# Optimization experiments

Hardware: AMD Instinct MI355X
Metric: run time of the kernel (lower is better)

Reference implementation:

```python
import jax, jax.numpy as jnp
import numpy as np

B, H, W = 8, 64, 64
EMBED, HEADS, HEAD_DIM = 768, 12, 64
FF = 3072
WS = 14  # window size
SCALE = HEAD_DIM ** -0.5
EPS = 1e-6


def setup_inputs() -> dict:
    key = jax.random.key(0)
    ks = jax.random.split(key, 8)
    def n(k, shp, s=0.02):
        return jax.random.normal(k, shp, jnp.float32) * s
    return {
        "x": jax.random.normal(ks[0], (B, H, W, EMBED), jnp.float32),
        "g1": jnp.ones((EMBED,), jnp.float32),
        "beta1": jnp.zeros((EMBED,), jnp.float32),
        "w_qkv": n(ks[1], (EMBED, 3 * EMBED)),
        "b_qkv": jnp.zeros((3 * EMBED,), jnp.float32),
        "w_proj": n(ks[2], (EMBED, EMBED)),
        "b_proj": jnp.zeros((EMBED,), jnp.float32),
        "rel_pos_h": n(ks[3], (2 * WS - 1, HEAD_DIM)),
        "rel_pos_w": n(ks[4], (2 * WS - 1, HEAD_DIM)),
        "g2": jnp.ones((EMBED,), jnp.float32),
        "beta2": jnp.zeros((EMBED,), jnp.float32),
        "w_fc1": n(ks[5], (EMBED, FF)),
        "b_fc1": jnp.zeros((FF,), jnp.float32),
        "w_fc2": n(ks[6], (FF, EMBED)),
        "b_fc2": jnp.zeros((EMBED,), jnp.float32),
    }


def layer_norm(x, g, b):
    m = jnp.mean(x, axis=-1, keepdims=True)
    v = jnp.mean(jnp.square(x - m), axis=-1, keepdims=True)
    return (x - m) * jax.lax.rsqrt(v + EPS) * g + b


def window_partition(x):
    b, h, w, c = x.shape
    ph, pw = (-h) % WS, (-w) % WS
    x = jnp.pad(x, ((0, 0), (0, ph), (0, pw), (0, 0)))
    hp, wp = h + ph, w + pw
    x = x.reshape(b, hp // WS, WS, wp // WS, WS, c)
    x = x.transpose(0, 1, 3, 2, 4, 5).reshape(-1, WS, WS, c)
    return x, (hp, wp)


def window_unpartition(win, pad_hw, hw):
    hp, wp = pad_hw
    h, w = hw
    b = win.shape[0] // ((hp // WS) * (wp // WS))
    x = win.reshape(b, hp // WS, wp // WS, WS, WS, -1)
    x = x.transpose(0, 1, 3, 2, 4, 5).reshape(b, hp, wp, -1)
    return x[:, :h, :w, :]


def attention(xw, w_qkv, b_qkv, w_proj, b_proj, rel_pos_h, rel_pos_w):
    bw, hs, ws_, c = xw.shape
    n = hs * ws_
    qkv = (xw.reshape(bw, n, c) @ w_qkv + b_qkv).reshape(bw, n, 3, HEADS, HEAD_DIM)
    q, k, v = jnp.moveaxis(qkv, 2, 0)            # each (bw, n, heads, hd)
    q = q.transpose(0, 2, 1, 3)                  # (bw, heads, n, hd)
    k = k.transpose(0, 2, 1, 3)
    v = v.transpose(0, 2, 1, 3)
    attn = jnp.einsum('bhnd,bhmd->bhnm', q * SCALE, k)
    # decomposed relative position bias (q unscaled, per torch reference)
    idx = jnp.arange(WS)[:, None] - jnp.arange(WS)[None, :] + (WS - 1)
    Rh = rel_pos_h[idx]                          # (ws, ws, hd)
    Rw = rel_pos_w[idx]
    r_q = q.reshape(bw, HEADS, WS, WS, HEAD_DIM)
    rel_h = jnp.einsum('bhpqd,pkd->bhpqk', r_q, Rh)
    rel_w = jnp.einsum('bhpqd,qkd->bhpqk', r_q, Rw)
    attn = attn.reshape(bw, HEADS, WS, WS, WS, WS)
    attn = attn + rel_h[..., :, None] + rel_w[..., None, :]
    attn = jax.nn.softmax(attn.reshape(bw, HEADS, n, n), axis=-1)
    out = jnp.einsum('bhnm,bhmd->bhnd', attn, v)
    out = out.transpose(0, 2, 1, 3).reshape(bw, hs, ws_, c)
    return out @ w_proj + b_proj


def reference(x, g1, beta1, w_qkv, b_qkv, w_proj, b_proj, rel_pos_h, rel_pos_w,
              g2, beta2, w_fc1, b_fc1, w_fc2, b_fc2):
    shortcut = x
    h = layer_norm(x, g1, beta1)
    win, pad_hw = window_partition(h)
    a = attention(win, w_qkv, b_qkv, w_proj, b_proj, rel_pos_h, rel_pos_w)
    a = window_unpartition(a, pad_hw, (x.shape[1], x.shape[2]))
    x = shortcut + a
    h2 = layer_norm(x, g2, beta2)
    mlp = jax.nn.gelu(h2 @ w_fc1 + b_fc1, approximate=False) @ w_fc2 + b_fc2
    return x + mlp
```

## Files before the change

### kernel.cpp

```cpp
#include <hip/hip_runtime.h>
#include <cstdint>


typedef unsigned short u16;
typedef __attribute__((ext_vector_type(8))) short short8;
typedef __attribute__((ext_vector_type(4))) float f32x4;

__device__ __forceinline__ u16 f2b(float f) {
    union { float f; unsigned int i; } x; x.f = f;
    unsigned int u = x.i;
    return (u16)((u + 0x7fffu + ((u >> 16) & 1u)) >> 16);
}
__device__ __forceinline__ float b2f(u16 u) {
    union { unsigned int i; float f; } x; x.i = ((unsigned int)u) << 16; return x.f;
}

__device__ __forceinline__ void gload16(const u16* g, u16* l) {
    __builtin_amdgcn_global_load_lds(
        (const __attribute__((address_space(1))) unsigned int*)g,
        (__attribute__((address_space(3))) unsigned int*)l, 16, 0, 0);
}

__device__ __forceinline__ int xcd_swz(int bid, int nwg) {
    int q = nwg >> 3, r = nwg & 7;
    int x = bid & 7, lo = bid >> 3;
    return (x < r ? x * (q + 1) : r * (q + 1) + (x - r) * q) + lo;
}

__global__ __launch_bounds__(256) void transpose_k(
    const float* __restrict__ in, u16* __restrict__ out, int R, int C)
{
    __shared__ float tile[32][33];
    int bpc = C >> 5;
    int r0 = (blockIdx.x / bpc) << 5;
    int c0 = (blockIdx.x % bpc) << 5;
    int lx = threadIdx.x & 31, ly = threadIdx.x >> 5;
#pragma unroll
    for (int s = 0; s < 32; s += 8)
        tile[ly + s][lx] = in[(size_t)(r0 + ly + s) * C + c0 + lx];
    __syncthreads();
#pragma unroll
    for (int s = 0; s < 32; s += 8)
        out[(size_t)(c0 + ly + s) * R + r0 + lx] = f2b(tile[lx][ly + s]);
}

__global__ __launch_bounds__(256) void ln_kernel(
    const float* __restrict__ in, const float* __restrict__ g,
    const float* __restrict__ beta, u16* __restrict__ out, int windowed,
    int row_base)
{
    __shared__ float sbuf[4];
    int tid = threadIdx.x;
    size_t orow = (size_t)blockIdx.x * 768;
    size_t irow;
    if (windowed) {
        int r = row_base + blockIdx.x;
        int win = r / 196, t = r % 196;
        int p = t / 14, q = t % 14;
        int b = win / 25, wt = win % 25;
        int i = (wt / 5) * 14 + p, j = (wt % 5) * 14 + q;
        if (i >= 64 || j >= 64) {
            out[orow + tid] = 0; out[orow + tid + 256] = 0; out[orow + tid + 512] = 0;
            return;
        }
        irow = (((size_t)b * 64 + i) * 64 + j) * 768;
    } else {
        irow = (size_t)blockIdx.x * 768;
    }
    float v0 = in[irow + tid];
    float v1 = in[irow + tid + 256];
    float v2 = in[irow + tid + 512];
    float s = v0 + v1 + v2;
#pragma unroll
    for (int off = 32; off; off >>= 1) s += __shfl_xor(s, off, 64);
    if ((tid & 63) == 0) sbuf[tid >> 6] = s;
    __syncthreads();
    float mean = (sbuf[0] + sbuf[1] + sbuf[2] + sbuf[3]) * (1.f / 768.f);
    __syncthreads();
    float d0 = v0 - mean, d1 = v1 - mean, d2 = v2 - mean;
    float sq = d0 * d0 + d1 * d1 + d2 * d2;
#pragma unroll
    for (int off = 32; off; off >>= 1) sq += __shfl_xor(sq, off, 64);
    if ((tid & 63) == 0) sbuf[tid >> 6] = sq;
    __syncthreads();
    float var = (sbuf[0] + sbuf[1] + sbuf[2] + sbuf[3]) * (1.f / 768.f);
    float rs = rsqrtf(var + 1e-6f);
    out[orow + tid]       = f2b(d0 * rs * g[tid]       + beta[tid]);
    out[orow + tid + 256] = f2b(d1 * rs * g[tid + 256] + beta[tid + 256]);
    out[orow + tid + 512] = f2b(d2 * rs * g[tid + 512] + beta[tid + 512]);
}


__device__ __forceinline__ short8 ldsf(const u16* P, int r, int quad) {
    return *(const short8*)(P + r * 32 + ((quad ^ ((r >> 1) & 3)) << 3));
}

__device__ __forceinline__ void comp32(const u16* __restrict__ Ap,
                                       const u16* __restrict__ Bp,
                                       f32x4 (&acc)[8][4],
                                       int wr, int wc, int quad, int l16)
{
    short8 a[4], b[4];
#pragma unroll
    for (int n = 0; n < 2; n++) b[n] = ldsf(Bp, wc * 64 + n * 16 + l16, quad);
#pragma unroll
    for (int m = 0; m < 4; m++) a[m] = ldsf(Ap, wr * 128 + m * 16 + l16, quad);
    __builtin_amdgcn_s_setprio(1);
#pragma unroll
    for (int m = 0; m < 4; m++)
#pragma unroll
        for (int n = 0; n < 2; n++)
            acc[m][n] = __builtin_amdgcn_mfma_f32_16x16x32_bf16(
                a[m], b[n], acc[m][n], 0, 0, 0);
    __builtin_amdgcn_s_setprio(0);
#pragma unroll
    for (int n = 0; n < 2; n++) b[2 + n] = ldsf(Bp, wc * 64 + (2 + n) * 16 + l16, quad);
    __builtin_amdgcn_s_setprio(1);
#pragma unroll
    for (int m = 0; m < 4; m++)
#pragma unroll
        for (int n = 0; n < 2; n++)
            acc[m][2 + n] = __builtin_amdgcn_mfma_f32_16x16x32_bf16(
                a[m], b[2 + n], acc[m][2 + n], 0, 0, 0);
    __builtin_amdgcn_s_setprio(0);
#pragma unroll
    for (int m = 0; m < 4; m++) a[m] = ldsf(Ap, wr * 128 + 64 + m * 16 + l16, quad);
    __builtin_amdgcn_s_setprio(1);
#pragma unroll
    for (int m = 0; m < 4; m++)
#pragma unroll
        for (int n = 0; n < 2; n++)
            acc[4 + m][2 + n] = __builtin_amdgcn_mfma_f32_16x16x32_bf16(
                a[m], b[2 + n], acc[4 + m][2 + n], 0, 0, 0);
    __builtin_amdgcn_s_setprio(0);
    __builtin_amdgcn_s_setprio(1);
#pragma unroll
    for (int m = 0; m < 4; m++)
#pragma unroll
        for (int n = 0; n < 2; n++)
            acc[4 + m][n] = __builtin_amdgcn_mfma_f32_16x16x32_bf16(
                a[m], b[n], acc[4 + m][n], 0, 0, 0);
    __builtin_amdgcn_s_setprio(0);
}

#define STAGE4(SA, SB, TT)                                                 \
    if ((TT) < nt) {                                                       \
        const size_t kk = (size_t)((TT) << 5);                             \
        gload16(A  + aoff0 + kk, (SA) + wbase);                            \
        gload16(A  + aoff1 + kk, (SA) + 4096 + wbase);                     \
        gload16(Bt + boff0 + kk, (SB) + wbase);                            \
        gload16(Bt + boff1 + kk, (SB) + 4096 + wbase);                     \
    }

#define GSTEP(CA, CB, SA, SB, TT)                                          \
    {                                                                      \
        __builtin_amdgcn_sched_barrier(0);                                 \
        __builtin_amdgcn_s_barrier();    \
        __builtin_amdgcn_sched_barrier(0);                                 \
        STAGE4(SA, SB, (TT) + 3);                                          \
        __builtin_amdgcn_sched_barrier(0);                                 \
        {                                                                  \
            const int d = nt - 1 - (TT);                                   \
            if (d >= 3)      asm volatile("s_waitcnt vmcnt(12)" ::: "memory"); \
            else if (d == 2) asm volatile("s_waitcnt vmcnt(8)"  ::: "memory"); \
            else if (d == 1) asm volatile("s_waitcnt vmcnt(4)"  ::: "memory"); \
            else             asm volatile("s_waitcnt vmcnt(0)"  ::: "memory"); \
        }                                                                  \
        __builtin_amdgcn_sched_barrier(0);                                 \
        __builtin_amdgcn_s_barrier();    \
        __builtin_amdgcn_sched_barrier(0);                                 \
        comp32(CA, CB, acc, wr, wc, quad, l16);                            \
    }

template <int EPI>
__global__ __launch_bounds__(512) void gemm256(
    const u16* __restrict__ A, const u16* __restrict__ Bt,
    const float* __restrict__ bias, void* __restrict__ CoutV,
    const float* __restrict__ resid, int M, int N, int K, int row_base)
{
    __shared__ __align__(16) u16 As0[256 * 32];
    __shared__ __align__(16) u16 As1[256 * 32];
    __shared__ __align__(16) u16 As2[256 * 32];
    __shared__ __align__(16) u16 As3[256 * 32];
    __shared__ __align__(16) u16 Bs0[256 * 32];
    __shared__ __align__(16) u16 Bs1[256 * 32];
    __shared__ __align__(16) u16 Bs2[256 * 32];
    __shared__ __align__(16) u16 Bs3[256 * 32];

    const int tid = threadIdx.x;
    const int lane = tid & 63, wave = tid >> 6;
    const int wr = wave >> 2, wc = wave & 3;
    const int quad = lane >> 4, l16 = lane & 15;
    const int ntile = N / 256;
    const int swz = xcd_swz(blockIdx.x, gridDim.x);
    const int m0 = (swz / ntile) * 256;
    const int n0 = (swz % ntile) * 256;

    const int rA   = (wave << 4) + (lane >> 2);
    const int kcol = (((lane & 3) ^ ((rA >> 1) & 3)) << 3);
    const size_t aoff0 = (size_t)(m0 + rA) * K + kcol;
    const size_t aoff1 = aoff0 + (size_t)128 * K;
    const size_t boff0 = (size_t)(n0 + rA) * K + kcol;
    const size_t boff1 = boff0 + (size_t)128 * K;
    const int wbase = wave * 512;

    f32x4 acc[8][4] = {};
    const int nt = K >> 5;

    STAGE4(As0, Bs0, 0);
    STAGE4(As1, Bs1, 1);
    STAGE4(As2, Bs2, 2);

#pragma unroll 1
    for (int t = 0; t < nt; t += 4) {
        GSTEP(As0, Bs0, As3, Bs3, t);
        GSTEP(As1, Bs1, As0, Bs0, t + 1);
        GSTEP(As2, Bs2, As1, Bs1, t + 2);
        GSTEP(As3, Bs3, As2, Bs2, t + 3);
    }

#pragma unroll
    for (int mi = 0; mi < 8; mi++) {
#pragma unroll
        for (int ni = 0; ni < 4; ni++) {
            const int gn = n0 + wc * 64 + ni * 16 + l16;
            const float bv = bias[gn];
#pragma unroll
            for (int r = 0; r < 4; r++) {
                const int row = m0 + wr * 128 + mi * 16 + quad * 4 + r;
                if (row >= M) continue;
                float v = acc[mi][ni][r] + bv;
                if (EPI == 0) {
                    ((u16*)CoutV)[(size_t)row * N + gn] = f2b(v);
                } else if (EPI == 1) {
                    int grow = row_base + row;
                    int win = grow / 196, t = grow % 196;
                    int p = t / 14, q = t % 14;
                    int b_ = win / 25, wt = win % 25;
                    int i = (wt / 5) * 14 + p, j = (wt % 5) * 14 + q;
                    if (i < 64 && j < 64) {
                        size_t idx = (((size_t)b_ * 64 + i) * 64 + j) * 768 + gn;
                        ((float*)CoutV)[idx] = resid[idx] + v;
                    }
                } else if (EPI == 2) {
                    float gl = 0.5f * v * (1.0f + erff(v * 0.70710678118654752f));
                    ((u16*)CoutV)[(size_t)row * N + gn] = f2b(gl);
                } else {
                    size_t idx = (size_t)(row_base + row) * 768 + gn;
                    ((float*)CoutV)[idx] = resid[idx] + v;
                }
            }
        }
    }
}

#define AT_W 72
#define PB_W 40

__global__ __launch_bounds__(256) void attn_mfma(
    const u16* __restrict__ qkv,
    const float* __restrict__ relh, const float* __restrict__ relw,
    u16* __restrict__ out)
{
    __shared__ __align__(16) u16 pbuf[4][32 * PB_W];
    __shared__ __align__(16) u16 Kc[64 * AT_W];
    __shared__ __align__(16) u16 Vt[64 * AT_W];
    u16* rel_ext = &pbuf[0][0];

    const int nwg = gridDim.x;
    const int swzb = xcd_swz(blockIdx.x, nwg);
    const int win = swzb / 24, rem = swzb % 24;
    const int head = rem >> 1, half = rem & 1;
    const int row0 = half * 128;
    const int tid = threadIdx.x, lane = tid & 63, wave = tid >> 6;
    const int quad = lane >> 4, l16 = lane & 15;
    const size_t base = (size_t)win * 196 * 2304 + (size_t)head * 64;

    short8 qf[2][2];
#pragma unroll
    for (int mi = 0; mi < 2; mi++) {
        int tok = row0 + wave * 32 + mi * 16 + l16;
        int rt = tok < 196 ? tok : 195;
        const u16* qp = qkv + base + (size_t)rt * 2304 + quad * 8;
        qf[mi][0] = *(const short8*)(qp);
        qf[mi][1] = *(const short8*)(qp + 32);
    }

    for (int e = tid; e < 64 * 64; e += 256) {
        int rr = e >> 6, cc = e & 63;
        float v = 0.f;
        if (rr < 27)      v = 8.f * relh[rr * 64 + cc];
        else if (rr < 54) v = 8.f * relw[(rr - 27) * 64 + cc];
        Kc[rr * AT_W + cc] = f2b(v);
    }
    if (tid < 128) {
        u16* rp = rel_ext + tid * 32;
        uint4 z = make_uint4(0u, 0u, 0u, 0u);
        *(uint4*)(rp) = z; *(uint4*)(rp + 8) = z;
        *(uint4*)(rp + 16) = z; *(uint4*)(rp + 24) = z;
        rp[31] = f2b(-1e30f);
    }
    __syncthreads();

#pragma unroll
    for (int cb = 0; cb < 2; cb++) {
#pragma unroll
        for (int nt = 0; nt < 2; nt++) {
            const u16* kp_ = Kc + (cb * 32 + nt * 16 + l16) * AT_W + quad * 8;
            short8 b0 = *(const short8*)(kp_);
            short8 b1 = *(const short8*)(kp_ + 32);
            int i = cb * 32 + nt * 16 + l16;
#pragma unroll
            for (int mi = 0; mi < 2; mi++) {
                f32x4 c = {};
                c = __builtin_amdgcn_mfma_f32_16x16x32_bf16(qf[mi][0], b0, c, 0, 0, 0);
                c = __builtin_amdgcn_mfma_f32_16x16x32_bf16(qf[mi][1], b1, c, 0, 0, 0);
#pragma unroll
                for (int r = 0; r < 4; r++) {
                    int row = wave * 32 + mi * 16 + quad * 4 + r;
                    int grow = row0 + row;
                    int rowB = grow < 196 ? grow : 195;
                    int p = rowB / 14, qq = rowB % 14;
                    if (i < 27) {
                        int t = p + 13 - i;
                        if (t >= 0 && t < 14) rel_ext[row * 32 + t] = f2b(c[r]);
                    } else if (i < 54) {
                        int t = qq + 13 - (i - 27);
                        if (t >= 0 && t < 14) rel_ext[row * 32 + 14 + t] = f2b(c[r]);
                    }
                }
            }
        }
    }
    short8 qe[2];
#pragma unroll
    for (int mi = 0; mi < 2; mi++)
        qe[mi] = *(const short8*)(rel_ext + (wave * 32 + mi * 16 + l16) * 32 + quad * 8);

    f32x4 acc[2][4] = {};
    float ml_[2][4], ll_[2][4];
#pragma unroll
    for (int mi = 0; mi < 2; mi++)
#pragma unroll
        for (int r = 0; r < 4; r++) { ml_[mi][r] = -1e30f; ll_[mi][r] = 0.f; }

#pragma unroll 1
    for (int c = 0; c < 4; c++) {
        const int kbase = c * 64;
        __syncthreads();
        {
            int key = tid >> 2;
            int cg  = (tid & 3) << 4;
            int gk = kbase + key;
            uint4 k0 = make_uint4(0u,0u,0u,0u), k1 = k0, v0 = k0, v1 = k0;
            if (gk < 196) {
                const u16* kp_ = qkv + base + 768  + (size_t)gk * 2304 + cg;
                const u16* vp_ = qkv + base + 1536 + (size_t)gk * 2304 + cg;
                k0 = *(const uint4*)(kp_); k1 = *(const uint4*)(kp_ + 8);
                v0 = *(const uint4*)(vp_); v1 = *(const uint4*)(vp_ + 8);
            }
            *(uint4*)(Kc + key * AT_W + cg)     = k0;
            *(uint4*)(Kc + key * AT_W + cg + 8) = k1;
            union { uint4 u; u16 h[8]; } a, b; a.u = v0; b.u = v1;
#pragma unroll
            for (int i = 0; i < 8; i++) Vt[(cg + i) * AT_W + key] = a.h[i];
#pragma unroll
            for (int i = 0; i < 8; i++) Vt[(cg + 8 + i) * AT_W + key] = b.h[i];
        }
        __syncthreads();

        short8 bo[4];
        {
            const u16 one = 0x3F80;
#pragma unroll
            for (int nt = 0; nt < 4; nt++) {
                int key = kbase + nt * 16 + l16;
                int inval = key >= 196;
                int kp = key / 14, kq = key - kp * 14;
                union { short8 s; u16 h[8]; } u;
#pragma unroll
                for (int j = 0; j < 8; j++) {
                    int t = quad * 8 + j;
                    u16 v = 0;
                    if (!inval && t == kp) v = one;
                    if (!inval && t >= 14 && (t - 14) == kq) v = one;
                    if (inval && t == 31) v = one;
                    u.h[j] = v;
                }
                bo[nt] = u.s;
            }
        }

        f32x4 s23[2][2];
#pragma unroll
        for (int mi = 0; mi < 2; mi++) {
            f32x4 s[4];
            __builtin_amdgcn_s_setprio(1);
#pragma unroll
            for (int nt = 0; nt < 4; nt++) {
                const u16* kp_ = Kc + (nt * 16 + l16) * AT_W + quad * 8;
                short8 kf0 = *(const short8*)(kp_);
                short8 kf1 = *(const short8*)(kp_ + 32);
                f32x4 t = {};
                t = __builtin_amdgcn_mfma_f32_16x16x32_bf16(qf[mi][0], kf0, t, 0, 0, 0);
                t = __builtin_amdgcn_mfma_f32_16x16x32_bf16(qf[mi][1], kf1, t, 0, 0, 0);
                t = __builtin_amdgcn_mfma_f32_16x16x32_bf16(qe[mi],    bo[nt], t, 0, 0, 0);
                s[nt] = t * 0.125f;
            }
            __builtin_amdgcn_s_setprio(0);
#pragma unroll
            for (int r = 0; r < 4; r++) {
                float mx = fmaxf(fmaxf(s[0][r], s[1][r]), fmaxf(s[2][r], s[3][r]));
#pragma unroll
                for (int off = 8; off; off >>= 1) mx = fmaxf(mx, __shfl_xor(mx, off, 16));
                float mo = ml_[mi][r];
                float mn = fmaxf(mo, mx);
                float alpha = __expf(mo - mn);
                ml_[mi][r] = mn;
                float p0 = __expf(s[0][r] - mn), p1 = __expf(s[1][r] - mn);
                float p2 = __expf(s[2][r] - mn), p3 = __expf(s[3][r] - mn);
                float ps = (p0 + p1) + (p2 + p3);
#pragma unroll
                for (int off = 8; off; off >>= 1) ps += __shfl_xor(ps, off, 16);
                ll_[mi][r] = ll_[mi][r] * alpha + ps;
#pragma unroll
                for (int ni = 0; ni < 4; ni++) acc[mi][ni][r] *= alpha;
                s[0][r] = p0; s[1][r] = p1; s[2][r] = p2; s[3][r] = p3;
            }
#pragma unroll
            for (int nt = 0; nt < 2; nt++)
#pragma unroll
                for (int r = 0; r < 4; r++)
                    pbuf[wave][(mi * 16 + quad * 4 + r) * PB_W + nt * 16 + l16] = f2b(s[nt][r]);
            s23[mi][0] = s[2]; s23[mi][1] = s[3];
        }

        __builtin_amdgcn_s_setprio(1);
#pragma unroll
        for (int mi = 0; mi < 2; mi++) {
            short8 pf = *(const short8*)(pbuf[wave] + (mi * 16 + l16) * PB_W + quad * 8);
#pragma unroll
            for (int ni = 0; ni < 4; ni++) {
                short8 vfn = *(const short8*)(Vt + (ni * 16 + l16) * AT_W + quad * 8);
                acc[mi][ni] = __builtin_amdgcn_mfma_f32_16x16x32_bf16(pf, vfn, acc[mi][ni], 0, 0, 0);
            }
        }
        __builtin_amdgcn_s_setprio(0);
#pragma unroll
        for (int mi = 0; mi < 2; mi++)
#pragma unroll
            for (int h = 0; h < 2; h++)
#pragma unroll
                for (int r = 0; r < 4; r++)
                    pbuf[wave][(mi * 16 + quad * 4 + r) * PB_W + h * 16 + l16] = f2b(s23[mi][h][r]);
        __builtin_amdgcn_s_setprio(1);
#pragma unroll
        for (int mi = 0; mi < 2; mi++) {
            short8 pf = *(const short8*)(pbuf[wave] + (mi * 16 + l16) * PB_W + quad * 8);
#pragma unroll
            for (int ni = 0; ni < 4; ni++) {
                short8 vfn = *(const short8*)(Vt + (ni * 16 + l16) * AT_W + 32 + quad * 8);
                acc[mi][ni] = __builtin_amdgcn_mfma_f32_16x16x32_bf16(pf, vfn, acc[mi][ni], 0, 0, 0);
            }
        }
        __builtin_amdgcn_s_setprio(0);
    }

#pragma unroll
    for (int mi = 0; mi < 2; mi++)
#pragma unroll
        for (int r = 0; r < 4; r++) {
            int tok = row0 + wave * 32 + mi * 16 + quad * 4 + r;
            if (tok < 196) {
                float inv = 1.f / ll_[mi][r];
                size_t ob = (size_t)(win * 196 + tok) * 768 + head * 64;
#pragma unroll
                for (int ni = 0; ni < 4; ni++)
                    out[ob + ni * 16 + l16] = f2b(acc[mi][ni][r] * inv);
            }
        }
}

extern "C" void kernel_launch(void* const* d_in, const int* in_sizes, int n_in,
                              void* d_out, int out_size, void* d_ws, size_t ws_size,
                              hipStream_t stream)
{
    const float* x      = (const float*)d_in[0];
    const float* g1     = (const float*)d_in[1];
    const float* beta1  = (const float*)d_in[2];
    const float* w_qkv  = (const float*)d_in[3];
    const float* b_qkv  = (const float*)d_in[4];
    const float* w_proj = (const float*)d_in[5];
    const float* b_proj = (const float*)d_in[6];
    const float* rph    = (const float*)d_in[7];
    const float* rpw    = (const float*)d_in[8];
    const float* g2     = (const float*)d_in[9];
    const float* beta2  = (const float*)d_in[10];
    const float* w_fc1  = (const float*)d_in[11];
    const float* b_fc1  = (const float*)d_in[12];
    const float* w_fc2  = (const float*)d_in[13];
    const float* b_fc2  = (const float*)d_in[14];
    float* out = (float*)d_out;

    const size_t WT = 14155776;
    size_t b1 = 0, b2 = 0;
    int nc = 0, mc = 0;
    auto fits = [&](int a, int m) -> bool {
        size_t rows = (size_t)(200 / a) * 196, toks = (size_t)32768 / m;
        size_t bb1 = rows * 768 * 2 >= toks * 768 * 2 ? rows * 768 * 2 : toks * 768 * 2;
        size_t bb2 = rows * 2304 * 2 >= toks * 3072 * 2 ? rows * 2304 * 2 : toks * 3072 * 2;
        if (WT + bb1 + bb2 <= ws_size) { b1 = bb1; b2 = bb2; nc = a; mc = m; return true; }
        return false;
    };
    if (!fits(1, 1) && !fits(1, 2) && !fits(2, 2) && !fits(2, 4) && !fits(4, 4))
        return;

    char* ws = (char*)d_ws;
    u16* wt0 = (u16*)ws;
    u16* wt1 = wt0 + 2304 * 768;
    u16* wt2 = wt1 + 768 * 768;
    u16* wt3 = wt2 + 3072 * 768;
    u16* buf1 = (u16*)(ws + WT);
    u16* buf2 = (u16*)(ws + WT + b1);

    dim3 blk(256), blk5(512);

    transpose_k<<<(768/32)*(2304/32), blk, 0, stream>>>(w_qkv,  wt0, 768, 2304);
    transpose_k<<<(768/32)*(768/32),  blk, 0, stream>>>(w_proj, wt1, 768, 768);
    transpose_k<<<(768/32)*(3072/32), blk, 0, stream>>>(w_fc1,  wt2, 768, 3072);
    transpose_k<<<(3072/32)*(768/32), blk, 0, stream>>>(w_fc2,  wt3, 3072, 768);

    {
        const int nw = 200 / nc, rows = nw * 196;
        const int mt = (rows + 255) / 256;
        for (int c = 0; c < nc; c++) {
            const int rb = c * rows;
            ln_kernel<<<rows, blk, 0, stream>>>(x, g1, beta1, buf1, 1, rb);
            gemm256<0><<<dim3(mt * (2304/256)), blk5, 0, stream>>>(
                buf1, wt0, b_qkv, buf2, nullptr, rows, 2304, 768, 0);
            attn_mfma<<<nw * 24, blk, 0, stream>>>(buf2, rph, rpw, buf1);
            gemm256<1><<<dim3(mt * (768/256)), blk5, 0, stream>>>(
                buf1, wt1, b_proj, out, x, rows, 768, 768, rb);
        }
    }

    {
        const int tk = 32768 / mc;
        const int mt2 = (tk + 255) / 256;
        for (int c = 0; c < mc; c++) {
            const int rb = c * tk;
            ln_kernel<<<tk, blk, 0, stream>>>(
                out + (size_t)rb * 768, g2, beta2, buf1, 0, 0);
            gemm256<2><<<dim3(mt2 * (3072/256)), blk5, 0, stream>>>(
                buf1, wt2, b_fc1, buf2, nullptr, tk, 3072, 768, 0);
            gemm256<3><<<dim3(mt2 * (768/256)), blk5, 0, stream>>>(
                buf2, wt3, b_fc2, out, out, tk, 768, 3072, rb);
        }
    }
}
```

Before: 1.548 ms.

## Restructure GEMM main loop into 3-stage ping-pong with split A/B prefetch

Replaces the 4-buffer LDS pipeline with a 3-buffer one and splits each K-tile into two half-compute phases (rows 0-63 and 64-127 per wave). The A prefetch is issued before the first half and the B prefetch before the second, each separated by block barriers and explicit lgkmcnt/vmcnt waits. The aim is to interleave global-to-LDS loads with MFMA bursts more finely and to reduce the LDS footprint. In exchange it adds more barriers per tile and a shorter prefetch distance, and the loop stride of three assumes K/32 is divisible by three.

Result: no change. 1.533 ms (-1.0%).

```diff
diff --git a/kernel.cpp b/kernel.cpp
--- a/kernel.cpp
+++ b/kernel.cpp
@@ -95,81 +95,71 @@
     return *(const short8*)(P + r * 32 + ((quad ^ ((r >> 1) & 3)) << 3));
 }
 
-__device__ __forceinline__ void comp32(const u16* __restrict__ Ap,
-                                       const u16* __restrict__ Bp,
-                                       f32x4 (&acc)[8][4],
-                                       int wr, int wc, int quad, int l16)
-{
-    short8 a[4], b[4];
-#pragma unroll
-    for (int n = 0; n < 2; n++) b[n] = ldsf(Bp, wc * 64 + n * 16 + l16, quad);
-#pragma unroll
-    for (int m = 0; m < 4; m++) a[m] = ldsf(Ap, wr * 128 + m * 16 + l16, quad);
-    __builtin_amdgcn_s_setprio(1);
-#pragma unroll
-    for (int m = 0; m < 4; m++)
-#pragma unroll
-        for (int n = 0; n < 2; n++)
-            acc[m][n] = __builtin_amdgcn_mfma_f32_16x16x32_bf16(
-                a[m], b[n], acc[m][n], 0, 0, 0);
-    __builtin_amdgcn_s_setprio(0);
-#pragma unroll
-    for (int n = 0; n < 2; n++) b[2 + n] = ldsf(Bp, wc * 64 + (2 + n) * 16 + l16, quad);
-    __builtin_amdgcn_s_setprio(1);
-#pragma unroll
-    for (int m = 0; m < 4; m++)
-#pragma unroll
-        for (int n = 0; n < 2; n++)
-            acc[m][2 + n] = __builtin_amdgcn_mfma_f32_16x16x32_bf16(
-                a[m], b[2 + n], acc[m][2 + n], 0, 0, 0);
-    __builtin_amdgcn_s_setprio(0);
-#pragma unroll
-    for (int m = 0; m < 4; m++) a[m] = ldsf(Ap, wr * 128 + 64 + m * 16 + l16, quad);
-    __builtin_amdgcn_s_setprio(1);
-#pragma unroll
-    for (int m = 0; m < 4; m++)
-#pragma unroll
-        for (int n = 0; n < 2; n++)
-            acc[4 + m][2 + n] = __builtin_amdgcn_mfma_f32_16x16x32_bf16(
-                a[m], b[2 + n], acc[4 + m][2 + n], 0, 0, 0);
-    __builtin_amdgcn_s_setprio(0);
-    __builtin_amdgcn_s_setprio(1);
-#pragma unroll
-    for (int m = 0; m < 4; m++)
-#pragma unroll
-        for (int n = 0; n < 2; n++)
-            acc[4 + m][n] = __builtin_amdgcn_mfma_f32_16x16x32_bf16(
-                a[m], b[n], acc[4 + m][n], 0, 0, 0);
-    __builtin_amdgcn_s_setprio(0);
-}
-
-#define STAGE4(SA, SB, TT)                                                 \
-    if ((TT) < nt) {                                                       \
-        const size_t kk = (size_t)((TT) << 5);                             \
-        gload16(A  + aoff0 + kk, (SA) + wbase);                            \
-        gload16(A  + aoff1 + kk, (SA) + 4096 + wbase);                     \
-        gload16(Bt + boff0 + kk, (SB) + wbase);                            \
-        gload16(Bt + boff1 + kk, (SB) + 4096 + wbase);                     \
-    }
-
-#define GSTEP(CA, CB, SA, SB, TT)                                          \
-    {                                                                      \
-        __builtin_amdgcn_sched_barrier(0);                                 \
-        __builtin_amdgcn_s_barrier();    \
-        __builtin_amdgcn_sched_barrier(0);                                 \
-        STAGE4(SA, SB, (TT) + 3);                                          \
-        __builtin_amdgcn_sched_barrier(0);                                 \
-        {                                                                  \
-            const int d = nt - 1 - (TT);                                   \
-            if (d >= 3)      asm volatile("s_waitcnt vmcnt(12)" ::: "memory"); \
-            else if (d == 2) asm volatile("s_waitcnt vmcnt(8)"  ::: "memory"); \
-            else if (d == 1) asm volatile("s_waitcnt vmcnt(4)"  ::: "memory"); \
-            else             asm volatile("s_waitcnt vmcnt(0)"  ::: "memory"); \
-        }                                                                  \
-        __builtin_amdgcn_sched_barrier(0);                                 \
-        __builtin_amdgcn_s_barrier();    \
-        __builtin_amdgcn_sched_barrier(0);                                 \
-        comp32(CA, CB, acc, wr, wc, quad, l16);                            \
+#define MF(I, J, AA, BB) \
+    acc[I][J] = __builtin_amdgcn_mfma_f32_16x16x32_bf16(AA, BB, acc[I][J], 0, 0, 0)
+
+#define STAGE_A(SA, TT) {                                                   \
+        const size_t kk = (size_t)((TT) << 5);                              \
+        gload16(A + aoff0 + kk, (SA) + wbase);                              \
+        gload16(A + aoff1 + kk, (SA) + 4096 + wbase); }
+
+#define STAGE_B(SB, TT) {                                                   \
+        const size_t kk = (size_t)((TT) << 5);                              \
+        gload16(Bt + boff0 + kk, (SB) + wbase);                             \
+        gload16(Bt + boff1 + kk, (SB) + 4096 + wbase); }
+
+#define TILE(CA, CB, SA, SB, TT)                                            \
+    {                                                                       \
+                                                     \
+        short8 a0_ = ldsf(CA, wr128 + l16,       quad);                     \
+        short8 a1_ = ldsf(CA, wr128 + 16 + l16,  quad);                     \
+        short8 a2_ = ldsf(CA, wr128 + 32 + l16,  quad);                     \
+        short8 a3_ = ldsf(CA, wr128 + 48 + l16,  quad);                     \
+        short8 b0_ = ldsf(CB, wc64 + l16,        quad);                     \
+        short8 b1_ = ldsf(CB, wc64 + 16 + l16,   quad);                     \
+        short8 b2_ = ldsf(CB, wc64 + 32 + l16,   quad);                     \
+        short8 b3_ = ldsf(CB, wc64 + 48 + l16,   quad);                     \
+        if ((TT) + 2 < nt) STAGE_A(SA, (TT) + 2);                           \
+        __builtin_amdgcn_sched_barrier(0);                                  \
+        __builtin_amdgcn_s_barrier();                                       \
+        __builtin_amdgcn_sched_barrier(0);                                  \
+        asm volatile("s_waitcnt lgkmcnt(0)" ::: "memory");                  \
+        __builtin_amdgcn_sched_barrier(0);                                  \
+        __builtin_amdgcn_s_setprio(1);                                      \
+        MF(0,0,a0_,b0_); MF(1,0,a1_,b0_); MF(2,0,a2_,b0_); MF(3,0,a3_,b0_); \
+        MF(0,1,a0_,b1_); MF(1,1,a1_,b1_); MF(2,1,a2_,b1_); MF(3,1,a3_,b1_); \
+        MF(0,2,a0_,b2_); MF(1,2,a1_,b2_); MF(2,2,a2_,b2_); MF(3,2,a3_,b2_); \
+        MF(0,3,a0_,b3_); MF(1,3,a1_,b3_); MF(2,3,a2_,b3_); MF(3,3,a3_,b3_); \
+        __builtin_amdgcn_s_setprio(0);                                      \
+        __builtin_amdgcn_sched_barrier(0);                                  \
+        __builtin_amdgcn_s_barrier();                                       \
+        __builtin_amdgcn_sched_barrier(0);                                  \
+                                                     \
+        a0_ = ldsf(CA, wr128 + 64 + l16,  quad);                            \
+        a1_ = ldsf(CA, wr128 + 80 + l16,  quad);                            \
+        a2_ = ldsf(CA, wr128 + 96 + l16,  quad);                            \
+        a3_ = ldsf(CA, wr128 + 112 + l16, quad);                            \
+        if ((TT) + 2 < nt) STAGE_B(SB, (TT) + 2);                           \
+        __builtin_amdgcn_sched_barrier(0);                                  \
+        if ((TT) + 2 < nt) {                                                \
+            asm volatile("s_waitcnt vmcnt(4)" ::: "memory");                \
+        } else if ((TT) + 1 < nt) {                                         \
+            asm volatile("s_waitcnt vmcnt(0)" ::: "memory");                \
+        }                                                                   \
+        __builtin_amdgcn_sched_barrier(0);                                  \
+        __builtin_amdgcn_s_barrier();                                       \
+        __builtin_amdgcn_sched_barrier(0);                                  \
+        asm volatile("s_waitcnt lgkmcnt(0)" ::: "memory");                  \
+        __builtin_amdgcn_sched_barrier(0);                                  \
+        __builtin_amdgcn_s_setprio(1);                                      \
+        MF(4,0,a0_,b0_); MF(5,0,a1_,b0_); MF(6,0,a2_,b0_); MF(7,0,a3_,b0_); \
+        MF(4,1,a0_,b1_); MF(5,1,a1_,b1_); MF(6,1,a2_,b1_); MF(7,1,a3_,b1_); \
+        MF(4,2,a0_,b2_); MF(5,2,a1_,b2_); MF(6,2,a2_,b2_); MF(7,2,a3_,b2_); \
+        MF(4,3,a0_,b3_); MF(5,3,a1_,b3_); MF(6,3,a2_,b3_); MF(7,3,a3_,b3_); \
+        __builtin_amdgcn_s_setprio(0);                                      \
+        __builtin_amdgcn_sched_barrier(0);                                  \
+        __builtin_amdgcn_s_barrier();                                       \
+        __builtin_amdgcn_sched_barrier(0);                                  \
     }
 
 template <int EPI>
@@ -181,16 +171,15 @@
     __shared__ __align__(16) u16 As0[256 * 32];
     __shared__ __align__(16) u16 As1[256 * 32];
     __shared__ __align__(16) u16 As2[256 * 32];
-    __shared__ __align__(16) u16 As3[256 * 32];
     __shared__ __align__(16) u16 Bs0[256 * 32];
     __shared__ __align__(16) u16 Bs1[256 * 32];
     __shared__ __align__(16) u16 Bs2[256 * 32];
-    __shared__ __align__(16) u16 Bs3[256 * 32];
 
     const int tid = threadIdx.x;
     const int lane = tid & 63, wave = tid >> 6;
     const int wr = wave >> 2, wc = wave & 3;
     const int quad = lane >> 4, l16 = lane & 15;
+    const int wr128 = wr * 128, wc64 = wc * 64;
     const int ntile = N / 256;
     const int swz = xcd_swz(blockIdx.x, gridDim.x);
     const int m0 = (swz / ntile) * 256;
@@ -207,16 +196,19 @@
     f32x4 acc[8][4] = {};
     const int nt = K >> 5;
 
-    STAGE4(As0, Bs0, 0);
-    STAGE4(As1, Bs1, 1);
-    STAGE4(As2, Bs2, 2);
+    STAGE_A(As0, 0); STAGE_B(Bs0, 0);
+    STAGE_A(As1, 1); STAGE_B(Bs1, 1);
+    __builtin_amdgcn_sched_barrier(0);
+    asm volatile("s_waitcnt vmcnt(4)" ::: "memory");
+    __builtin_amdgcn_sched_barrier(0);
+    __builtin_amdgcn_s_barrier();
+    __builtin_amdgcn_sched_barrier(0);
 
 #pragma unroll 1
-    for (int t = 0; t < nt; t += 4) {
-        GSTEP(As0, Bs0, As3, Bs3, t);
-        GSTEP(As1, Bs1, As0, Bs0, t + 1);
-        GSTEP(As2, Bs2, As1, Bs1, t + 2);
-        GSTEP(As3, Bs3, As2, Bs2, t + 3);
+    for (int t = 0; t < nt; t += 3) {
+        TILE(As0, Bs0, As2, Bs2, t);
+        TILE(As1, Bs1, As0, Bs0, t + 1);
+        TILE(As2, Bs2, As1, Bs1, t + 2);
     }
 
 #pragma unroll
```
